# Optimization experiments

Hardware: AMD Instinct MI355X
Metric: run time of the kernel (lower is better)

## Reference

```python
import jax, jax.numpy as jnp
import numpy as np

E = 16          # num_experts
D_FULL = 1024   # full_feature_dim
DM = 128        # expert_dim
S = D_FULL // E # per-expert feature slice = 64
P = 2048        # num patches
B = 8
C = 256
W = 3           # local_window (neighbor experts)
DEPTH = 8       # cantor_depth
NEG = -1e9


def _cantor_coord(pos, max_len, depth):
    x = pos / max(1, max_len - 1)
    x = max(1e-6, min(x, 1.0 - 1e-6))
    val, factor = 0.0, 0.5
    for _ in range(depth):
        x *= 3.0
        d = int(x)
        x -= d
        if d == 2:
            val += factor
        factor *= 0.5
    return val


def _expert_routes():
    coords = np.array([_cantor_coord(i, E, DEPTH) for i in range(E)], dtype=np.float32)
    return np.stack([np.argsort(np.abs(coords - coords[i]), kind='stable')[:W] for i in range(E)]).astype(np.int32)


ROUTES = _expert_routes()  # [E, W] static routing table


def setup_inputs():
    key = jax.random.key(0)
    ks = jax.random.split(key, 8)
    h = S // 4
    lim = float(np.sqrt(6.0 / (S + DM)))  # xavier_uniform bound
    penta = jax.random.normal(ks[5], (E, 5, DM), jnp.float32) * 0.02
    penta = penta / jnp.linalg.norm(penta, axis=-1, keepdims=True)
    return {
        'tokens': jax.random.normal(ks[0], (B, P, D_FULL), jnp.float32),
        'fingerprints': jax.random.uniform(ks[1], (P,), jnp.float32),
        'alpha': jnp.ones((E,), jnp.float32),
        'gate_w1': jax.random.normal(ks[2], (E, S, h), jnp.float32) * 0.05,
        'gate_b1': jnp.zeros((E, h), jnp.float32),
        'gate_w2': jax.random.normal(ks[3], (E, h, 1), jnp.float32) * 0.05,
        'gate_b2': jnp.zeros((E, 1), jnp.float32),
        'q_w': jax.random.uniform(ks[4], (E, S, DM), jnp.float32, -lim, lim),
        'k_w': jax.random.uniform(ks[6], (E, S, DM), jnp.float32, -lim, lim),
        'v_w': jax.random.uniform(ks[7], (E, S, DM), jnp.float32, -lim, lim),
        'penta': penta,
        'fusion_w': jnp.ones((5,), jnp.float32) / 5.0,
        'temperature': jnp.float32(0.5),
    }


def _dispatch(fingerprints):
    # Fingerprint band masks, then fixed-capacity gather (static shapes for jit).
    masks = []
    for e in range(E):
        lo, hi = e / E, (e + 1) / E
        m = (fingerprints >= lo) & ((fingerprints <= hi) if e == E - 1 else (fingerprints < hi))
        masks.append(m)
    masks = jnp.stack(masks)                             # [E, P]
    order = jnp.argsort(jnp.where(masks, 0, 1), axis=1)  # stable: assigned patches first
    idx = order[:, :C]                                   # [E, C]
    valid = jnp.take_along_axis(masks, idx, axis=1)      # [E, C]
    return idx, valid


def _forward(tokens, fingerprints, alpha, gate_w1, gate_b1, gate_w2, gate_b2,
             q_w, k_w, v_w, penta, fusion_w, temperature):
    idx, valid = _dispatch(fingerprints)
    Kaff, Qaff, Vs = [], [], []
    for e in range(E):  # fixed structural loop over experts
        feats = tokens[:, idx[e], e * S:(e + 1) * S]                       # [B, C, S]
        g = jax.nn.sigmoid(jax.nn.gelu(feats @ gate_w1[e] + gate_b1[e]) @ gate_w2[e] + gate_b2[e])
        aw = jax.nn.sigmoid(alpha[e])
        feats = feats * (g * aw + (1.0 - aw))                              # gated features
        Q = feats @ q_w[e]
        K = feats @ k_w[e]
        V = feats @ v_w[e]                                                 # [B, C, DM]
        dirs = penta[e] / jnp.linalg.norm(penta[e], axis=-1, keepdims=True)  # [5, DM]
        Kaff.append(jnp.einsum('bcd,vd->vbc', K, dirs))
        Qaff.append(jnp.einsum('bcd,vd->vbc', Q, dirs))
        Vs.append(V)
    Kaff = jnp.stack(Kaff)   # [E, 5, B, C]
    Qaff = jnp.stack(Qaff)   # [E, 5, B, C]
    Vs = jnp.stack(Vs)       # [E, B, C, DM]
    wdir = jax.nn.softmax(fusion_w)
    vmask = valid.astype(jnp.float32)
    out = jnp.zeros((B, P, DM), jnp.float32)
    for e in range(E):
        nb = ROUTES[e]                                  # static [W]
        Knb, Vnb, vnb = Kaff[nb], Vs[nb], vmask[nb]     # [W,5,B,C], [W,B,C,DM], [W,C]
        scores = jnp.einsum('vbi,nvbj->vbinj', Qaff[e], Knb) / temperature
        scores = jnp.where(vnb[None, None, None, :, :] > 0, scores, NEG)
        attn = jax.nn.softmax(scores.reshape(5, B, C, W * C), axis=-1).reshape(5, B, C, W, C)
        att = jnp.einsum('vbinj,nbjd->vbid', attn, Vnb)  # per-direction attended values
        out_e = jnp.einsum('v,vbid->bid', wdir, att) * vmask[e][None, :, None]
        out = out.at[:, idx[e]].add(out_e)              # scatter back to patch positions
    return out


def reference(tokens, fingerprints, alpha, gate_w1, gate_b1, gate_w2, gate_b2,
              q_w, k_w, v_w, penta, fusion_w, temperature):
    return _forward(tokens, fingerprints, alpha, gate_w1, gate_b1, gate_w2, gate_b2,
                    q_w, k_w, v_w, penta, fusion_w, temperature)
```

## Files before the change

### kernel.cpp

```cpp
#include <hip/hip_runtime.h>
#include <cfloat>
#include <math.h>

#define E 16
#define DFULL 1024
#define DM 128
#define S 64
#define P 2048
#define B 8
#define C 256
#define W 3
#define H 16
#define RQ 16
#define NCH 16
#define LOG2E 1.4426950408889634f
#define WST 272

typedef __attribute__((ext_vector_type(8))) short short8;
typedef __attribute__((ext_vector_type(4))) float f32x4;
#define MFMA_BF16(a, b, c) __builtin_amdgcn_mfma_f32_16x16x32_bf16((a), (b), (c), 0, 0, 0)

struct RoutesArg { int nb[E][W]; };

static void compute_routes(int r[E][W]) {
  float coords[E];
  for (int i = 0; i < E; ++i) {
    double x = (double)i / (double)(E - 1);
    if (x < 1e-06) x = 1e-06;
    if (x > 1.0 - 1e-06) x = 1.0 - 1e-06;
    double val = 0.0, factor = 0.5;
    for (int k = 0; k < 8; ++k) {
      x *= 3.0;
      int d = (int)x;
      x -= (double)d;
      if (d == 2) val += factor;
      factor *= 0.5;
    }
    coords[i] = (float)val;
  }
  for (int e = 0; e < E; ++e) {
    float de[E];
    for (int i = 0; i < E; ++i) de[i] = fabsf(coords[i] - coords[e]);
    bool used[E] = {false};
    for (int w = 0; w < W; ++w) {
      int best = -1; float bd = FLT_MAX;
      for (int i = 0; i < E; ++i)
        if (!used[i] && de[i] < bd) { bd = de[i]; best = i; }
      used[best] = true;
      r[e][w] = best;
    }
  }
}

__device__ __forceinline__ unsigned short bfhi(float x) {
  return (unsigned short)(__float_as_uint(x) >> 16);
}
__device__ __forceinline__ float bf2f(unsigned short h) {
  return __uint_as_float(((unsigned)h) << 16);
}
__device__ __forceinline__ float gelu_tanh(float x) {
  float x3 = x * x * x;
  return 0.5f * x * (1.0f + tanhf(0.7978845608028654f * (x + 0.044715f * x3)));
}
__device__ __forceinline__ float sigmoidf_(float x) {
  return 1.0f / (1.0f + __expf(-x));
}

__global__ __launch_bounds__(256) void k_setup(
    const float* __restrict__ fp, const float* __restrict__ qw,
    const float* __restrict__ kw, const float* __restrict__ penta,
    const float* __restrict__ temp, const float* __restrict__ vw,
    int* __restrict__ idx, int* __restrict__ counts,
    unsigned short* __restrict__ qkdT_h, unsigned short* __restrict__ qkdT_l,
    unsigned short* __restrict__ vwT_h, unsigned short* __restrict__ vwT_l) {
  int e = blockIdx.x, t = threadIdx.x;
  __shared__ float s_tr[DM * 65];
  if (blockIdx.y == 1) {
    const float* vwe = vw + (size_t)e * S * DM;
    for (int u = t; u < S * DM; u += 256) {
      int s = u >> 7, d = u & 127;
      s_tr[d * 65 + s] = vwe[u];
    }
    __syncthreads();
    for (int u = t; u < S * DM; u += 256) {
      int d = u >> 6, s = u & 63;
      float f = s_tr[d * 65 + s];
      unsigned short h = bfhi(f), l = bfhi(f - bf2f(h));
      vwT_h[(size_t)e * 8192 + u] = h;
      vwT_l[(size_t)e * 8192 + u] = l;
    }
    return;
  }
  {
    float lo = (float)e * 0.0625f, hi = (float)(e + 1) * 0.0625f;
    bool last = (e == E - 1);
    int p0 = t * 8;
    int m[8]; int ls = 0;
    #pragma unroll
    for (int k = 0; k < 8; ++k) {
      float f = fp[p0 + k];
      bool mm = (f >= lo) && (last ? (f <= hi) : (f < hi));
      m[k] = mm ? 1 : 0;
      ls += m[k];
    }
    __shared__ int sc[256];
    sc[t] = ls;
    __syncthreads();
    for (int o = 1; o < 256; o <<= 1) {
      int v = (t >= o) ? sc[t - o] : 0;
      __syncthreads();
      sc[t] += v;
      __syncthreads();
    }
    int incl = sc[t];
    int M = sc[255];
    int r = incl - ls;
    #pragma unroll
    for (int k = 0; k < 8; ++k) {
      if (m[k]) {
        if (r < C) idx[e * C + r] = p0 + k;
        r++;
      }
    }
    if (t == 0) counts[e] = (M < C) ? M : C;
  }
  __syncthreads();
  __shared__ float s_rn[5];
  if (t < 5) {
    const float* pv = penta + (e * 5 + t) * DM;
    float ss = 0.f;
    for (int d = 0; d < DM; ++d) ss += pv[d] * pv[d];
    s_rn[t] = 1.0f / sqrtf(ss);
  }
  __syncthreads();
  float invT = 1.0f / temp[0];
  int s = t & 63, cg = t >> 6;
  for (int c = cg; c < 10; c += 4) {
    int v = c % 5;
    bool isq = (c < 5);
    const float* wrow = (isq ? qw : kw) + ((size_t)e * S + s) * DM;
    const float* pv = penta + (e * 5 + v) * DM;
    float acc = 0.f;
    #pragma unroll
    for (int d4 = 0; d4 < DM / 4; ++d4) {
      float4 a = ((const float4*)wrow)[d4];
      float4 p = ((const float4*)pv)[d4];
      acc += a.x * p.x + a.y * p.y + a.z * p.z + a.w * p.w;
    }
    float val = acc * s_rn[v] * (isq ? invT : 1.0f);
    unsigned short h = bfhi(val), l = bfhi(val - bf2f(h));
    qkdT_h[(e * 16 + c) * 64 + s] = h;
    qkdT_l[(e * 16 + c) * 64 + s] = l;
  }
  for (int c = 10 + cg; c < 16; c += 4) {
    qkdT_h[(e * 16 + c) * 64 + s] = 0;
    qkdT_l[(e * 16 + c) * 64 + s] = 0;
  }
}

__global__ __launch_bounds__(512, 8) void k_p1(
    const float* __restrict__ tokens, const float* __restrict__ alpha,
    const float* __restrict__ gw1, const float* __restrict__ gb1,
    const float* __restrict__ gw2, const float* __restrict__ gb2,
    const unsigned short* __restrict__ qkdT_h, const unsigned short* __restrict__ qkdT_l,
    const unsigned short* __restrict__ vwT_h, const unsigned short* __restrict__ vwT_l,
    const int* __restrict__ idx, const int* __restrict__ counts,
    float* __restrict__ Qa, float* __restrict__ Ka,
    unsigned short* __restrict__ Vt_h, unsigned short* __restrict__ Vt_l,
    float* __restrict__ kmx, float* __restrict__ kmn,
    float* __restrict__ out) {
  int e = blockIdx.x, b = blockIdx.y, rq = blockIdx.z;
  int t = threadIdx.x;

  {
    int blk = (e * B + b) * NCH + rq;
    if (t < 256) {
      float4 z4 = {0.f, 0.f, 0.f, 0.f};
      ((float4*)out)[(size_t)blk * 256 + t] = z4;
    }
  }

  int Me = counts[e];
  int r0 = rq * RQ;
  if (r0 >= Me) {
    if (t < 5) {
      kmx[((e * 5 + t) * B + b) * NCH + rq] = -FLT_MAX;
      kmn[((e * 5 + t) * B + b) * NCH + rq] = FLT_MAX;
    }
    return;
  }

  __shared__ float s_f[RQ * 65];
  __shared__ __align__(16) unsigned short s_fh[RQ * 72];
  __shared__ __align__(16) unsigned short s_fl[RQ * 72];
  __shared__ float s_gw1[S * H];
  __shared__ float s_gh[RQ * 8 * H];
  __shared__ float s_scl[RQ];
  __shared__ float s_kx[5 * RQ], s_kn[5 * RQ];
  __shared__ __align__(16) unsigned short s_vth[DM * 16];
  __shared__ __align__(16) unsigned short s_vtl[DM * 16];

  if (t < 256) {
    int row = t >> 4, q4 = t & 15;
    int ii = r0 + row;
    int pos = (ii < Me) ? idx[e * C + ii] : idx[e * C];
    const float* trow = tokens + ((size_t)b * P + pos) * DFULL + e * S;
    float4 v4 = ((const float4*)trow)[q4];
    s_f[row * 65 + q4 * 4 + 0] = v4.x;
    s_f[row * 65 + q4 * 4 + 1] = v4.y;
    s_f[row * 65 + q4 * 4 + 2] = v4.z;
    s_f[row * 65 + q4 * 4 + 3] = v4.w;
    ((float4*)s_gw1)[t] = ((const float4*)(gw1 + (size_t)e * S * H))[t];
  }
  __syncthreads();

  if (t < 128) {
    int row = t >> 3, sq = t & 7;
    float hh[H];
    #pragma unroll
    for (int j = 0; j < H; ++j) hh[j] = 0.f;
    #pragma unroll
    for (int k = 0; k < 8; ++k) {
      int s = sq * 8 + k;
      float fs = s_f[row * 65 + s];
      const float* gr = s_gw1 + s * H;
      #pragma unroll
      for (int j = 0; j < H; ++j) hh[j] += fs * gr[j];
    }
    #pragma unroll
    for (int j = 0; j < H; ++j) s_gh[(row * 8 + sq) * H + j] = hh[j];
  }
  __syncthreads();
  if (t < RQ) {
    float z = gb2[e];
    #pragma unroll
    for (int j = 0; j < H; ++j) {
      float hj = gb1[e * H + j];
      #pragma unroll
      for (int p = 0; p < 8; ++p) hj += s_gh[(t * 8 + p) * H + j];
      z += gelu_tanh(hj) * gw2[e * H + j];
    }
    float aw = sigmoidf_(alpha[e]);
    s_scl[t] = sigmoidf_(z) * aw + (1.0f - aw);
  }
  __syncthreads();
  if (t < 256) {
    int row = t >> 4, s0 = (t & 15) * 4;
    float sc = s_scl[row];
    #pragma unroll
    for (int k = 0; k < 4; ++k) {
      float f = s_f[row * 65 + s0 + k] * sc;
      unsigned short h = bfhi(f), l = bfhi(f - bf2f(h));
      s_fh[row * 72 + s0 + k] = h;
      s_fl[row * 72 + s0 + k] = l;
    }
  }
  __syncthreads();

  int L = t & 63, wv = t >> 6, quad = L >> 4, col = L & 15;

  {
    const unsigned short* vTh = vwT_h + (size_t)e * 8192;
    const unsigned short* vTl = vwT_l + (size_t)e * 8192;
    f32x4 va = {0.f, 0.f, 0.f, 0.f};
    int d0 = wv * 16 + col;
    #pragma unroll
    for (int kc = 0; kc < 2; ++kc) {
      int ko = kc * 32 + quad * 8;
      short8 ah = *(const short8*)(s_fh + col * 72 + ko);
      short8 al = *(const short8*)(s_fl + col * 72 + ko);
      short8 bh = *(const short8*)(vTh + d0 * 64 + ko);
      short8 bl = *(const short8*)(vTl + d0 * 64 + ko);
      va = MFMA_BF16(ah, bh, va);
      va = MFMA_BF16(ah, bl, va);
      va = MFMA_BF16(al, bh, va);
    }
    #pragma unroll
    for (int reg = 0; reg < 4; ++reg) {
      int row = quad * 4 + reg;
      float f0 = va[reg];
      unsigned short h0 = bfhi(f0), l0 = bfhi(f0 - bf2f(h0));
      s_vth[d0 * 16 + row] = h0;
      s_vtl[d0 * 16 + row] = l0;
    }
  }

  if (wv == 0) {
    const unsigned short* qTh = qkdT_h + e * 16 * 64;
    const unsigned short* qTl = qkdT_l + e * 16 * 64;
    f32x4 qa = {0.f, 0.f, 0.f, 0.f};
    #pragma unroll
    for (int kc = 0; kc < 2; ++kc) {
      int ko = kc * 32 + quad * 8;
      short8 ah = *(const short8*)(s_fh + col * 72 + ko);
      short8 al = *(const short8*)(s_fl + col * 72 + ko);
      short8 bh = *(const short8*)(qTh + col * 64 + ko);
      short8 bl = *(const short8*)(qTl + col * 64 + ko);
      qa = MFMA_BF16(ah, bh, qa);
      qa = MFMA_BF16(ah, bl, qa);
      qa = MFMA_BF16(al, bh, qa);
    }
    #pragma unroll
    for (int reg = 0; reg < 4; ++reg) {
      int row = quad * 4 + reg;
      int ii = r0 + row;
      float val = qa[reg];
      if (col < 5) {
        if (ii < Me) Qa[((e * 5 + col) * B + b) * C + ii] = val;
      } else if (col < 10) {
        int v = col - 5;
        if (ii < Me) Ka[((e * 5 + v) * B + b) * C + ii] = val;
        s_kx[v * RQ + row] = (ii < Me) ? val : -FLT_MAX;
        s_kn[v * RQ + row] = (ii < Me) ? val : FLT_MAX;
      }
    }
  }
  __syncthreads();
  if (t < 5) {
    float mx = -FLT_MAX, mn = FLT_MAX;
    for (int r = 0; r < RQ; ++r) {
      mx = fmaxf(mx, s_kx[t * RQ + r]);
      mn = fminf(mn, s_kn[t * RQ + r]);
    }
    kmx[((e * 5 + t) * B + b) * NCH + rq] = mx;
    kmn[((e * 5 + t) * B + b) * NCH + rq] = mn;
  }
  if (t < 256) {
    size_t base = (size_t)(e * B + b) * (DM * C);
    int jsl = t >> 7, d = t & 127;
    size_t dst = base + ((size_t)(rq * 2 + jsl) * DM + d) * 8;
    int src = d * 16 + jsl * 8;
    *(short8*)(Vt_h + dst) = *(const short8*)(s_vth + src);
    *(short8*)(Vt_l + dst) = *(const short8*)(s_vtl + src);
  }
}

__global__ __launch_bounds__(512, 8) void k_p2v(
    const float* __restrict__ Qa, const float* __restrict__ Ka,
    const unsigned short* __restrict__ Vt_h, const unsigned short* __restrict__ Vt_l,
    const float* __restrict__ kmx, const float* __restrict__ kmn,
    const int* __restrict__ idx, const int* __restrict__ counts,
    const float* __restrict__ fusw, float* __restrict__ out, RoutesArg R) {
  int e = blockIdx.x, b = blockIdx.y, rq = blockIdx.z;
  int t = threadIdx.x;
  int Me = counts[e];
  int r0 = rq * RQ;
  if (r0 >= Me) return;

  __shared__ float s_ka[5 * C];
  __shared__ __align__(16) unsigned short s_wh[RQ * WST];
  __shared__ __align__(16) unsigned short s_wl[RQ * WST];
  __shared__ float s_lp[32 * 5 * RQ];
  __shared__ float s_KX[5], s_KN[5];
  __shared__ float s_l[5 * RQ];
  float* s_red = (float*)s_wh;

  int nbs[3] = {R.nb[e][0], R.nb[e][1], R.nb[e][2]};
  int Mns[3] = {counts[nbs[0]], counts[nbs[1]], counts[nbs[2]]};
  int row = t & 15, jq = t >> 4;
  int ii = r0 + row;

  if (t < 240) {
    int v = t / 48, rr = t % 48, n = rr >> 4, k = rr & 15;
    int base = ((nbs[n] * 5 + v) * B + b) * NCH + k;
    s_red[t] = kmx[base];
    s_red[240 + t] = kmn[base];
  }
  __syncthreads();
  if (t < 5) {
    float KX = -FLT_MAX, KN = FLT_MAX;
    for (int u = 0; u < 48; ++u) {
      KX = fmaxf(KX, s_red[t * 48 + u]);
      KN = fminf(KN, s_red[240 + t * 48 + u]);
    }
    s_KX[t] = KX; s_KN[t] = KN;
  }
  __syncthreads();

  float q2[5], m2[5];
  #pragma unroll
  for (int v = 0; v < 5; ++v) {
    float qv = Qa[(((size_t)e * 5 + v) * B + b) * C + ii];
    q2[v] = qv * LOG2E;
    m2[v] = ((qv > 0.f) ? qv * s_KX[v] : qv * s_KN[v]) * LOG2E;
  }

  float lp[5] = {0.f, 0.f, 0.f, 0.f, 0.f};
  for (int n = 0; n < 3; ++n) {
    __syncthreads();
    if (t < 320) {
      int v = t >> 6, off = t & 63;
      ((float4*)s_ka)[v * 64 + off] =
          ((const float4*)(Ka + (((size_t)nbs[n] * 5 + v) * B + b) * C))[off];
    }
    __syncthreads();
    int Mn = Mns[n];
    for (int j = jq; j < Mn; j += 32) {
      #pragma unroll
      for (int v = 0; v < 5; ++v)
        lp[v] += exp2f(fmaf(q2[v], s_ka[v * C + j], -m2[v]));
    }
  }
  #pragma unroll
  for (int v = 0; v < 5; ++v) s_lp[(jq * 5 + v) * RQ + row] = lp[v];
  __syncthreads();
  if (t < 80) {
    int v = t >> 4, rw = t & 15;
    float l = 0.f;
    #pragma unroll
    for (int g = 0; g < 32; ++g) l += s_lp[(g * 5 + v) * RQ + rw];
    s_l[v * RQ + rw] = l;
  }
  __syncthreads();

  float fw[5];
  #pragma unroll
  for (int v = 0; v < 5; ++v) fw[v] = fusw[v];
  float fmx = fw[0];
  #pragma unroll
  for (int v = 1; v < 5; ++v) fmx = fmaxf(fmx, fw[v]);
  float fsum = 0.f;
  #pragma unroll
  for (int v = 0; v < 5; ++v) { fw[v] = __expf(fw[v] - fmx); fsum += fw[v]; }
  float c2[5];
  #pragma unroll
  for (int v = 0; v < 5; ++v) {
    float cl = (fw[v] / fsum) / s_l[v * RQ + row];
    c2[v] = __log2f(cl) - m2[v];
  }

  int L = t & 63, wv = t >> 6, quad = L >> 4, col = L & 15;
  int d0 = wv * 16 + col;
  f32x4 acc = {0.f, 0.f, 0.f, 0.f};

  for (int n = 0; n < 3; ++n) {
    int ne = nbs[n], Mn = Mns[n];
    __syncthreads();
    if (t < 320) {
      int v = t >> 6, off = t & 63;
      ((float4*)s_ka)[v * 64 + off] =
          ((const float4*)(Ka + (((size_t)ne * 5 + v) * B + b) * C))[off];
    }
    __syncthreads();
    {
      short8 wh8, wl8;
      #pragma unroll
      for (int k2 = 0; k2 < 8; ++k2) {
        int jj = jq * 8 + k2;
        float ww = 0.f;
        if (jj < Mn) {
          #pragma unroll
          for (int v = 0; v < 5; ++v)
            ww += exp2f(fmaf(q2[v], s_ka[v * C + jj], c2[v]));
        }
        unsigned short h = bfhi(ww), l = bfhi(ww - bf2f(h));
        wh8[k2] = (short)h;
        wl8[k2] = (short)l;
      }
      *(short8*)(s_wh + row * WST + jq * 8) = wh8;
      *(short8*)(s_wl + row * WST + jq * 8) = wl8;
    }
    __syncthreads();
    const unsigned short* vbh = Vt_h + (size_t)(ne * B + b) * (DM * C);
    const unsigned short* vbl = Vt_l + (size_t)(ne * B + b) * (DM * C);
    int kcN = (Mn + 31) >> 5;
    for (int kc = 0; kc < kcN; ++kc) {
      int ko = kc * 32 + quad * 8;
      short8 ah = *(const short8*)(s_wh + col * WST + ko);
      short8 al = *(const short8*)(s_wl + col * WST + ko);
      size_t sb = ((size_t)(kc * 4 + quad) * DM + d0) * 8;
      short8 bh = *(const short8*)(vbh + sb);
      short8 bl = *(const short8*)(vbl + sb);
      acc = MFMA_BF16(ah, bh, acc);
      acc = MFMA_BF16(ah, bl, acc);
      acc = MFMA_BF16(al, bh, acc);
    }
  }

  #pragma unroll
  for (int reg = 0; reg < 4; ++reg) {
    int rr = quad * 4 + reg;
    int iw = r0 + rr;
    if (iw < Me) {
      int pos = idx[e * C + iw];
      out[((size_t)b * P + pos) * DM + d0] = acc[reg];
    }
  }
}

extern "C" void kernel_launch(void* const* d_in, const int* in_sizes, int n_in,
                              void* d_out, int out_size, void* d_ws, size_t ws_size,
                              hipStream_t stream) {
  const float* tokens = (const float*)d_in[0];
  const float* fingerprints = (const float*)d_in[1];
  const float* alpha = (const float*)d_in[2];
  const float* gw1 = (const float*)d_in[3];
  const float* gb1 = (const float*)d_in[4];
  const float* gw2 = (const float*)d_in[5];
  const float* gb2 = (const float*)d_in[6];
  const float* qw = (const float*)d_in[7];
  const float* kw = (const float*)d_in[8];
  const float* vw = (const float*)d_in[9];
  const float* penta = (const float*)d_in[10];
  const float* fusw = (const float*)d_in[11];
  const float* temp = (const float*)d_in[12];
  float* out = (float*)d_out;

  float* ws = (float*)d_ws;
  float* Qa = ws;
  float* Ka = Qa + (size_t)E * 5 * B * C;
  float* kmx = Ka + (size_t)E * 5 * B * C;
  float* kmn = kmx + (size_t)E * 5 * B * NCH;
  unsigned short* qkdT_h = (unsigned short*)(kmn + (size_t)E * 5 * B * NCH);
  unsigned short* qkdT_l = qkdT_h + (size_t)E * 16 * 64;
  unsigned short* vwT_h = qkdT_l + (size_t)E * 16 * 64;
  unsigned short* vwT_l = vwT_h + (size_t)E * S * DM;
  unsigned short* Vt_h = vwT_l + (size_t)E * S * DM;
  unsigned short* Vt_l = Vt_h + (size_t)E * B * DM * C;
  int* idx = (int*)(Vt_l + (size_t)E * B * DM * C);
  int* counts = idx + (size_t)E * C;

  RoutesArg R;
  compute_routes(R.nb);

  k_setup<<<dim3(E, 2), dim3(256), 0, stream>>>(fingerprints, qw, kw, penta, temp, vw,
                                                idx, counts, qkdT_h, qkdT_l, vwT_h, vwT_l);
  k_p1<<<dim3(E, B, NCH), dim3(512), 0, stream>>>(tokens, alpha, gw1, gb1, gw2, gb2,
                                                  qkdT_h, qkdT_l, vwT_h, vwT_l,
                                                  idx, counts, Qa, Ka, Vt_h, Vt_l,
                                                  kmx, kmn, out);
  k_p2v<<<dim3(E, B, NCH), dim3(512), 0, stream>>>(Qa, Ka, Vt_h, Vt_l, kmx, kmn,
                                                   idx, counts, fusw, out, R);
}
```

Measured before the change: 191.9 us.

## Preload all neighbor keys, use wave-shuffle reductions, and prefetch V tiles

The p2v kernel now loads all three neighbor key blocks into shared memory once, instead of reloading them with extra barriers in each pass. The key-bound and partial-sum reductions use wave shuffles in place of shared-memory scans. The weight-building loop computes only the chunks that are actually used, and the loop over V tiles prefetches the next global bf16 fragment before issuing the MFMAs. Fast exp2, fdividef and an exp-based tanh replace the precise intrinsics, which costs some numerical accuracy and uses more shared memory.

```diff
diff --git a/kernel.cpp b/kernel.cpp
--- a/kernel.cpp
+++ b/kernel.cpp
@@ -17,8 +17,15 @@
 #define WST 272
 
 typedef __attribute__((ext_vector_type(8))) short short8;
+typedef __attribute__((ext_vector_type(4))) short short4v;
 typedef __attribute__((ext_vector_type(4))) float f32x4;
 #define MFMA_BF16(a, b, c) __builtin_amdgcn_mfma_f32_16x16x32_bf16((a), (b), (c), 0, 0, 0)
+
+#if defined(__HIP_DEVICE_COMPILE__) && __has_builtin(__builtin_amdgcn_exp2f)
+#define EXP2(x) __builtin_amdgcn_exp2f(x)
+#else
+#define EXP2(x) exp2f(x)
+#endif
 
 struct RoutesArg { int nb[E][W]; };
 
@@ -59,11 +66,13 @@
   return __uint_as_float(((unsigned)h) << 16);
 }
 __device__ __forceinline__ float gelu_tanh(float x) {
-  float x3 = x * x * x;
-  return 0.5f * x * (1.0f + tanhf(0.7978845608028654f * (x + 0.044715f * x3)));
+  float u = 0.7978845608028654f * (x + 0.044715f * x * x * x);
+  float ez = __expf(2.0f * u);
+  float th = 1.0f - __fdividef(2.0f, ez + 1.0f);
+  return 0.5f * x * (1.0f + th);
 }
 __device__ __forceinline__ float sigmoidf_(float x) {
-  return 1.0f / (1.0f + __expf(-x));
+  return __fdividef(1.0f, 1.0f + __expf(-x));
 }
 
 __global__ __launch_bounds__(256) void k_setup(
@@ -347,33 +356,40 @@
   int r0 = rq * RQ;
   if (r0 >= Me) return;
 
-  __shared__ float s_ka[5 * C];
+  __shared__ __align__(16) float s_ka[3 * 5 * C];
   __shared__ __align__(16) unsigned short s_wh[RQ * WST];
   __shared__ __align__(16) unsigned short s_wl[RQ * WST];
-  __shared__ float s_lp[32 * 5 * RQ];
+  __shared__ float s_lp[8 * 5 * RQ];
   __shared__ float s_KX[5], s_KN[5];
   __shared__ float s_l[5 * RQ];
-  float* s_red = (float*)s_wh;
 
   int nbs[3] = {R.nb[e][0], R.nb[e][1], R.nb[e][2]};
   int Mns[3] = {counts[nbs[0]], counts[nbs[1]], counts[nbs[2]]};
   int row = t & 15, jq = t >> 4;
   int ii = r0 + row;
-
-  if (t < 240) {
-    int v = t / 48, rr = t % 48, n = rr >> 4, k = rr & 15;
-    int base = ((nbs[n] * 5 + v) * B + b) * NCH + k;
-    s_red[t] = kmx[base];
-    s_red[240 + t] = kmn[base];
-  }
-  __syncthreads();
-  if (t < 5) {
+  int L = t & 63, wv = t >> 6, quad = L >> 4, col = L & 15;
+
+  for (int u = t; u < 960; u += 512) {
+    int n = (u >= 640) ? 2 : ((u >= 320) ? 1 : 0);
+    int r2 = u - n * 320;
+    int v = r2 >> 6, off = r2 & 63;
+    ((float4*)s_ka)[n * 320 + (v << 6) + off] =
+        ((const float4*)(Ka + (((size_t)nbs[n] * 5 + v) * B + b) * C))[off];
+  }
+  if (wv < 5) {
     float KX = -FLT_MAX, KN = FLT_MAX;
-    for (int u = 0; u < 48; ++u) {
-      KX = fmaxf(KX, s_red[t * 48 + u]);
-      KN = fminf(KN, s_red[240 + t * 48 + u]);
-    }
-    s_KX[t] = KX; s_KN[t] = KN;
+    if (L < 48) {
+      int n = L >> 4, k = L & 15;
+      int base = ((nbs[n] * 5 + wv) * B + b) * NCH + k;
+      KX = kmx[base];
+      KN = kmn[base];
+    }
+    #pragma unroll
+    for (int off = 32; off; off >>= 1) {
+      KX = fmaxf(KX, __shfl_xor(KX, off));
+      KN = fminf(KN, __shfl_xor(KN, off));
+    }
+    if (L == 0) { s_KX[wv] = KX; s_KN[wv] = KN; }
   }
   __syncthreads();
 
@@ -387,28 +403,29 @@
 
   float lp[5] = {0.f, 0.f, 0.f, 0.f, 0.f};
   for (int n = 0; n < 3; ++n) {
-    __syncthreads();
-    if (t < 320) {
-      int v = t >> 6, off = t & 63;
-      ((float4*)s_ka)[v * 64 + off] =
-          ((const float4*)(Ka + (((size_t)nbs[n] * 5 + v) * B + b) * C))[off];
-    }
-    __syncthreads();
+    const float* ka_n = s_ka + n * 1280;
     int Mn = Mns[n];
     for (int j = jq; j < Mn; j += 32) {
       #pragma unroll
       for (int v = 0; v < 5; ++v)
-        lp[v] += exp2f(fmaf(q2[v], s_ka[v * C + j], -m2[v]));
-    }
-  }
-  #pragma unroll
-  for (int v = 0; v < 5; ++v) s_lp[(jq * 5 + v) * RQ + row] = lp[v];
+        lp[v] += EXP2(fmaf(q2[v], ka_n[v * C + j], -m2[v]));
+    }
+  }
+  #pragma unroll
+  for (int v = 0; v < 5; ++v) {
+    lp[v] += __shfl_xor(lp[v], 16);
+    lp[v] += __shfl_xor(lp[v], 32);
+  }
+  if (L < 16) {
+    #pragma unroll
+    for (int v = 0; v < 5; ++v) s_lp[(wv * 5 + v) * RQ + L] = lp[v];
+  }
   __syncthreads();
   if (t < 80) {
     int v = t >> 4, rw = t & 15;
     float l = 0.f;
     #pragma unroll
-    for (int g = 0; g < 32; ++g) l += s_lp[(g * 5 + v) * RQ + rw];
+    for (int w = 0; w < 8; ++w) l += s_lp[(w * 5 + v) * RQ + rw];
     s_l[v * RQ + rw] = l;
   }
   __syncthreads();
@@ -422,58 +439,60 @@
   float fsum = 0.f;
   #pragma unroll
   for (int v = 0; v < 5; ++v) { fw[v] = __expf(fw[v] - fmx); fsum += fw[v]; }
+  float rfs = __fdividef(1.0f, fsum);
   float c2[5];
   #pragma unroll
   for (int v = 0; v < 5; ++v) {
-    float cl = (fw[v] / fsum) / s_l[v * RQ + row];
+    float cl = __fdividef(fw[v] * rfs, s_l[v * RQ + row]);
     c2[v] = __log2f(cl) - m2[v];
   }
 
-  int L = t & 63, wv = t >> 6, quad = L >> 4, col = L & 15;
   int d0 = wv * 16 + col;
   f32x4 acc = {0.f, 0.f, 0.f, 0.f};
 
   for (int n = 0; n < 3; ++n) {
     int ne = nbs[n], Mn = Mns[n];
+    int kcN = (Mn + 31) >> 5;
+    const float* ka_n = s_ka + n * 1280;
     __syncthreads();
-    if (t < 320) {
-      int v = t >> 6, off = t & 63;
-      ((float4*)s_ka)[v * 64 + off] =
-          ((const float4*)(Ka + (((size_t)ne * 5 + v) * B + b) * C))[off];
-    }
-    __syncthreads();
-    {
-      short8 wh8, wl8;
+    int jlim = kcN * 32;
+    for (int j0 = jq * 4; j0 < jlim; j0 += 128) {
+      short4v h4, l4;
       #pragma unroll
-      for (int k2 = 0; k2 < 8; ++k2) {
-        int jj = jq * 8 + k2;
+      for (int k2 = 0; k2 < 4; ++k2) {
+        int jj = j0 + k2;
         float ww = 0.f;
         if (jj < Mn) {
           #pragma unroll
           for (int v = 0; v < 5; ++v)
-            ww += exp2f(fmaf(q2[v], s_ka[v * C + jj], c2[v]));
+            ww += EXP2(fmaf(q2[v], ka_n[v * C + jj], c2[v]));
         }
         unsigned short h = bfhi(ww), l = bfhi(ww - bf2f(h));
-        wh8[k2] = (short)h;
-        wl8[k2] = (short)l;
+        h4[k2] = (short)h;
+        l4[k2] = (short)l;
       }
-      *(short8*)(s_wh + row * WST + jq * 8) = wh8;
-      *(short8*)(s_wl + row * WST + jq * 8) = wl8;
+      *(short4v*)(s_wh + row * WST + j0) = h4;
+      *(short4v*)(s_wl + row * WST + j0) = l4;
     }
     __syncthreads();
     const unsigned short* vbh = Vt_h + (size_t)(ne * B + b) * (DM * C);
     const unsigned short* vbl = Vt_l + (size_t)(ne * B + b) * (DM * C);
-    int kcN = (Mn + 31) >> 5;
+    size_t sb0 = ((size_t)quad * DM + d0) * 8;
+    short8 bh = *(const short8*)(vbh + sb0);
+    short8 bl = *(const short8*)(vbl + sb0);
     for (int kc = 0; kc < kcN; ++kc) {
+      int kn = (kc + 1 < kcN) ? (kc + 1) : kc;
+      size_t sb = ((size_t)(kn * 4 + quad) * DM + d0) * 8;
+      short8 nbh = *(const short8*)(vbh + sb);
+      short8 nbl = *(const short8*)(vbl + sb);
       int ko = kc * 32 + quad * 8;
       short8 ah = *(const short8*)(s_wh + col * WST + ko);
       short8 al = *(const short8*)(s_wl + col * WST + ko);
-      size_t sb = ((size_t)(kc * 4 + quad) * DM + d0) * 8;
-      short8 bh = *(const short8*)(vbh + sb);
-      short8 bl = *(const short8*)(vbl + sb);
       acc = MFMA_BF16(ah, bh, acc);
       acc = MFMA_BF16(ah, bl, acc);
       acc = MFMA_BF16(al, bh, acc);
+      bh = nbh;
+      bl = nbl;
     }
   }
 
```

Measured after the change: 177.2 us. -7.7%, faster.
